# Kernel tuning notes

Measured on AMD Instinct MI355X. Metric: run time of the kernel, lower is better.

Reference implementation:

```python
import jax, jax.numpy as jnp
import numpy as np

B, N, D, H, HID = 8, 729, 1152, 12, 4304
HD = D // H
EPS = 1e-6


def _layer_norm(x, g, b):
    mu = jnp.mean(x, axis=-1, keepdims=True)
    var = jnp.mean((x - mu) ** 2, axis=-1, keepdims=True)
    return (x - mu) / jnp.sqrt(var + EPS) * g + b


def setup_inputs() -> dict:
    key = jax.random.key(0)
    ks = jax.random.split(key, 9)
    s = 0.02
    return {
        "x": jax.random.normal(ks[0], (B, N, D), jnp.float32),
        "wq": jax.random.normal(ks[1], (D, D), jnp.float32) * s,
        "bq": jnp.zeros((D,), jnp.float32),
        "wk": jax.random.normal(ks[2], (D, D), jnp.float32) * s,
        "bk": jnp.zeros((D,), jnp.float32),
        "wv": jax.random.normal(ks[3], (D, D), jnp.float32) * s,
        "bv": jnp.zeros((D,), jnp.float32),
        "wo": jax.random.normal(ks[4], (D, D), jnp.float32) * s,
        "bo": jnp.zeros((D,), jnp.float32),
        "ln1_g": jnp.ones((D,), jnp.float32),
        "ln1_b": jnp.zeros((D,), jnp.float32),
        "w_fc1": jax.random.normal(ks[5], (HID, D), jnp.float32) * s,
        "b_fc1": jnp.zeros((HID,), jnp.float32),
        "w_fc2": jax.random.normal(ks[6], (D, HID), jnp.float32) * s,
        "b_fc2": jnp.zeros((D,), jnp.float32),
        "ln2_g": jnp.ones((D,), jnp.float32),
        "ln2_b": jnp.zeros((D,), jnp.float32),
    }


def reference(x, wq, bq, wk, bk, wv, bv, wo, bo, ln1_g, ln1_b,
              w_fc1, b_fc1, w_fc2, b_fc2, ln2_g, ln2_b):
    b, n, d = x.shape
    # split_heads in the source is a plain view (B, H, N, HD) -- NOT a transpose.
    def heads(t):
        return t.reshape(b, H, n, HD)

    Q = heads(x @ wq.T + bq)
    K = heads(x @ wk.T + bk)
    V = heads(x @ wv.T + bv)

    scores = jnp.einsum("bhqd,bhkd->bhqk", Q, K) * (HD ** -0.5)
    attn_w = jax.nn.softmax(scores, axis=-1)
    o = jnp.einsum("bhqk,bhkd->bhqd", attn_w, V)  # [B,H,N,HD]
    o = jnp.swapaxes(o, 1, 2).reshape(b, n, d)
    attn_out = o @ wo.T + bo

    # post-norm: LN(sublayer) + residual
    h = _layer_norm(attn_out, ln1_g, ln1_b) + x

    # quirky MLP: activation applied BEFORE fc1 (faithful to source)
    m = jax.nn.gelu(h, approximate=True)
    m = m @ w_fc1.T + b_fc1
    m = m @ w_fc2.T + b_fc2

    return _layer_norm(m, ln2_g, ln2_b) + h
```

## Files before the change

### kernel.cpp

```cpp
#include <hip/hip_runtime.h>
#include <hip/hip_bf16.h>

#define BF16 __hip_bfloat16

typedef short short8 __attribute__((ext_vector_type(8)));
typedef short short4v __attribute__((ext_vector_type(4)));
typedef float v4f __attribute__((ext_vector_type(4)));
typedef float f4 __attribute__((ext_vector_type(4)));

__device__ float g_bp[1152];
__device__ BF16  g_wm[1152 * 1152];

__device__ __forceinline__ short f2bs(float f) {
    __hip_bfloat16 h = __float2bfloat16(f);
    return *(short*)&h;
}

__device__ __forceinline__ float bs2f(short s) {
    __hip_bfloat16 h = *(__hip_bfloat16*)&s;
    return __bfloat162float(h);
}

__device__ __forceinline__ void async_cp16(const BF16* g, BF16* l) {
    __builtin_amdgcn_global_load_lds(
        (const __attribute__((address_space(1))) void*)g,
        (__attribute__((address_space(3))) void*)l,
        16, 0, 0);
}

__device__ __forceinline__ int xcd_chunk(int u, int nwg) {
    int xcd = u & 7, i = u >> 3;
    int q = nwg >> 3, r = nwg & 7;
    return (xcd < r ? xcd * (q + 1) : r * (q + 1) + (xcd - r) * q) + i;
}

__global__ __launch_bounds__(256) void prep_kernel(
    const float* __restrict__ wq, const float* __restrict__ wk,
    const float* __restrict__ wv, const float* __restrict__ wo,
    const float* __restrict__ wfc1, const float* __restrict__ wfc2,
    const float* __restrict__ x,
    const float* __restrict__ bfc1, const float* __restrict__ bfc2,
    BF16* __restrict__ wbq, BF16* __restrict__ wbk,
    BF16* __restrict__ wbv, BF16* __restrict__ wbo,
    BF16* __restrict__ wbf1t, BF16* __restrict__ wbf2,
    BF16* __restrict__ xb)
{
    __shared__ float tile[64][65];
    const int bid = blockIdx.x;
    const int tid = threadIdx.x;

    if (bid < 16641) {
        const int i = bid * 256 + tid;
        constexpr int N_DD  = 331776;
        constexpr int N4    = 4 * N_DD;
        constexpr int N_F2  = 1253376;
        constexpr int E_F2  = N4 + N_F2;
        constexpr int N_X   = 1679616;
        constexpr int TOTAL = E_F2 + N_X;

        if (i < N4) {
            int seg = i / N_DD, j = i - seg * N_DD;
            const float* s = (seg == 0) ? wq : (seg == 1) ? wk : (seg == 2) ? wv : wo;
            BF16* d = (seg == 0) ? wbq : (seg == 1) ? wbk : (seg == 2) ? wbv : wbo;
            f4 v = ((const f4*)s)[j];
            short4v o = {f2bs(v.x), f2bs(v.y), f2bs(v.z), f2bs(v.w)};
            ((short4v*)d)[j] = o;
        } else if (i < E_F2) {
            int j = i - N4;
            int row = j / 1088;
            int c = (j - row * 1088) * 4;
            short4v o = {0, 0, 0, 0};
            if (c < 4304) {
                f4 v = *(const f4*)(wfc2 + (size_t)row * 4304 + c);
                o[0] = f2bs(v.x); o[1] = f2bs(v.y); o[2] = f2bs(v.z); o[3] = f2bs(v.w);
            }
            *(short4v*)(wbf2 + (size_t)row * 4352 + c) = o;
        } else if (i < TOTAL) {
            int j = i - E_F2;
            f4 v = ((const f4*)x)[j];
            short4v o = {f2bs(v.x), f2bs(v.y), f2bs(v.z), f2bs(v.w)};
            ((short4v*)xb)[j] = o;
        }
    } else if (bid < 17865) {
        const int b2 = bid - 16641;
        const int h0 = (b2 % 68) * 64;
        const int d0 = (b2 / 68) * 64;
#pragma unroll
        for (int i = 0; i < 4; ++i) {
            int lin = tid + i * 256;
            int r = lin >> 4, c4 = lin & 15;
            f4 v = {0.f, 0.f, 0.f, 0.f};
            if (h0 + r < 4304)
                v = *(const f4*)(wfc1 + (size_t)(h0 + r) * 1152 + d0 + c4 * 4);
            tile[r][c4 * 4 + 0] = v.x;
            tile[r][c4 * 4 + 1] = v.y;
            tile[r][c4 * 4 + 2] = v.z;
            tile[r][c4 * 4 + 3] = v.w;
        }
        __syncthreads();
#pragma unroll
        for (int i = 0; i < 2; ++i) {
            int lin = tid + i * 256;
            int dr = lin >> 3, h8 = lin & 7;
            short8 o;
#pragma unroll
            for (int e = 0; e < 8; ++e)
                o[e] = f2bs(tile[h8 * 8 + e][dr]);
            *(short8*)(wbf1t + (size_t)(d0 + dr) * 4352 + h0 + h8 * 8) = o;
        }
    } else {
        const int row = (bid - 17865) * 4 + (tid >> 6);
        const int lane = tid & 63;
        const float* wr = wfc2 + (size_t)row * 4304;
        float s = 0.f;
        for (int k = lane; k < 4304; k += 64) s += wr[k] * bfc1[k];
#pragma unroll
        for (int mm = 1; mm < 64; mm <<= 1) s += __shfl_xor(s, mm, 64);
        if (lane == 0) g_bp[row] = s + bfc2[row];
    }
}

__global__ __launch_bounds__(512, 2) void qkv_wm8_kernel(
    const BF16* __restrict__ A,
    const BF16* __restrict__ Wqkv,
    const float* __restrict__ b0, const float* __restrict__ b1,
    const float* __restrict__ b2,
    BF16* __restrict__ C, size_t cstride, int M,
    const BF16* __restrict__ W2,
    const BF16* __restrict__ W1t,
    float* __restrict__ P)
{
    __shared__ __align__(16) BF16 smem[65536];
    const int bid  = blockIdx.x;
    const int tid  = threadIdx.x;
    const int lane = tid & 63;
    const int wave = tid >> 6;
    const int quad = lane >> 4;
    const int l16  = lane & 15;
    const v4f zf = {0.f, 0.f, 0.f, 0.f};

    int rr[2], sw[2], lo[2];
#pragma unroll
    for (int j = 0; j < 2; ++j) {
        int c = tid + j * 512;
        rr[j] = c >> 3;
        sw[j] = (((c & 7) - (c >> 3)) & 7) << 3;
        lo[j] = (c & ~63) * 8;
    }

    if (bid < 162) {
        BF16* Am = smem;
        BF16* Bm = smem + 8192;
        const int mz  = bid / 81;
        const int idx = bid - mz * 81;
        const int m0 = (idx % 9) * 128;
        const int n0 = (idx / 9) * 128;
        const int ks0 = mz * 34;
        const int wm = (wave >> 1) * 32;
        const int wn = (wave & 1) * 64;

        v4f acc[2][4];
#pragma unroll
        for (int i = 0; i < 2; ++i)
#pragma unroll
            for (int j = 0; j < 4; ++j) acc[i][j] = zf;

        const BF16* gA[2]; const BF16* gB[2];
#pragma unroll
        for (int j = 0; j < 2; ++j) {
            gA[j] = W2 + (size_t)(m0 + rr[j]) * 4352 + ks0 * 64 + sw[j];
            gB[j] = W1t + (size_t)(n0 + rr[j]) * 4352 + ks0 * 64 + sw[j];
        }

        for (int kt = 0; kt < 34; ++kt) {
#pragma unroll
            for (int j = 0; j < 2; ++j) { async_cp16(gA[j], Am + lo[j]); gA[j] += 64; }
#pragma unroll
            for (int j = 0; j < 2; ++j) { async_cp16(gB[j], Bm + lo[j]); gB[j] += 64; }
            __syncthreads();
#pragma unroll
            for (int ks = 0; ks < 2; ++ks) {
                short8 af[2], bfg[4];
#pragma unroll
                for (int mt = 0; mt < 2; ++mt) {
                    int row = wm + mt * 16 + l16;
                    af[mt] = *(const short8*)(Am + row * 64 + ((((ks << 2) | quad) + row & 7) & 7) * 8);
                }
#pragma unroll
                for (int nt = 0; nt < 4; ++nt) {
                    int row = wn + nt * 16 + l16;
                    bfg[nt] = *(const short8*)(Bm + row * 64 + ((((ks << 2) | quad) + row & 7) & 7) * 8);
                }
#pragma unroll
                for (int mt = 0; mt < 2; ++mt)
#pragma unroll
                    for (int nt = 0; nt < 4; ++nt)
                        acc[mt][nt] = __builtin_amdgcn_mfma_f32_16x16x32_bf16(
                            af[mt], bfg[nt], acc[mt][nt], 0, 0, 0);
            }
            __syncthreads();
        }

        float* Pz = P + (size_t)mz * 1327104;
#pragma unroll
        for (int mt = 0; mt < 2; ++mt)
#pragma unroll
            for (int nt = 0; nt < 4; ++nt)
#pragma unroll
                for (int r2 = 0; r2 < 4; ++r2) {
                    int row = m0 + wm + mt * 16 + quad * 4 + r2;
                    int col = n0 + wn + nt * 16 + l16;
                    Pz[(size_t)row * 1152 + col] = acc[mt][nt][r2];
                }
    } else {
        const int wg = xcd_chunk(bid - 162, 322);
        const int m0 = (wg / 14) * 256;
        const int n0 = (wg % 14) * 256;
        const int wr = wave >> 2;
        const int wc = wave & 3;
        BF16* As = smem;
        BF16* Bs = smem + 32768;

        v4f acc[8][4];
#pragma unroll
        for (int i = 0; i < 8; ++i)
#pragma unroll
            for (int j = 0; j < 4; ++j) acc[i][j] = zf;

        #define STAGE_A(dd, hh, tt)                                            \
            {                                                                  \
                _Pragma("unroll")                                              \
                for (int j = 0; j < 2; ++j)                                    \
                    async_cp16(A + (size_t)(m0 + (hh) * 128 + rr[j]) * 1152    \
                                 + (tt) * 64 + sw[j],                          \
                               As + (dd) * 16384 + (hh) * 8192 + lo[j]);       \
            }
        #define STAGE_B(dd, hh, tt)                                            \
            {                                                                  \
                _Pragma("unroll")                                              \
                for (int j = 0; j < 2; ++j)                                    \
                    async_cp16(Wqkv + (size_t)(n0 + (hh) * 128 + rr[j]) * 1152 \
                                 + (tt) * 64 + sw[j],                          \
                               Bs + (dd) * 16384 + (hh) * 8192 + lo[j]);       \
            }

        STAGE_B(0, 0, 0); STAGE_B(0, 1, 0);
        STAGE_A(0, 0, 0); STAGE_A(0, 1, 0);
        STAGE_B(1, 0, 1); STAGE_B(1, 1, 1);
        asm volatile("s_waitcnt vmcnt(4)" ::: "memory");
        __builtin_amdgcn_s_barrier();
        __builtin_amdgcn_sched_barrier(0);

        short8 bfr[4][2], afr[2][2];
#pragma unroll 2
        for (int it = 0; it < 18; ++it) {
            const int d = it & 1;
            const BF16* Ad = As + d * 16384;
            const BF16* Bd = Bs + d * 16384;
#pragma unroll
            for (int q = 0; q < 4; ++q) {
                if (q == 0) {
#pragma unroll
                    for (int nt = 0; nt < 4; ++nt) {
                        int R = wc * 64 + nt * 16 + l16;
#pragma unroll
                        for (int ks = 0; ks < 2; ++ks)
                            bfr[nt][ks] = *(const short8*)(
                                Bd + R * 64 + ((((ks << 2) | quad) + R & 7) & 7) * 8);
                    }
                }
#pragma unroll
                for (int mi = 0; mi < 2; ++mi) {
                    int R = wr * 128 + (q * 2 + mi) * 16 + l16;
#pragma unroll
                    for (int ks = 0; ks < 2; ++ks)
                        afr[mi][ks] = *(const short8*)(
                            Ad + R * 64 + ((((ks << 2) | quad) + R & 7) & 7) * 8);
                }
                if (q == 0) { if (it + 1 < 18) STAGE_A(d ^ 1, 0, it + 1); }
                if (q == 1) { if (it + 1 < 18) STAGE_A(d ^ 1, 1, it + 1); }
                if (q == 2) { if (it + 2 < 18) STAGE_B(d,     0, it + 2); }
                if (q == 3) { if (it + 2 < 18) STAGE_B(d,     1, it + 2); }

                __builtin_amdgcn_s_barrier();
                asm volatile("s_waitcnt lgkmcnt(0)" ::: "memory");
                __builtin_amdgcn_sched_barrier(0);
                __builtin_amdgcn_s_setprio(1);
#pragma unroll
                for (int ks = 0; ks < 2; ++ks)
#pragma unroll
                    for (int mi = 0; mi < 2; ++mi)
#pragma unroll
                        for (int nt = 0; nt < 4; ++nt)
                            acc[q * 2 + mi][nt] = __builtin_amdgcn_mfma_f32_16x16x32_bf16(
                                afr[mi][ks], bfr[nt][ks], acc[q * 2 + mi][nt], 0, 0, 0);
                __builtin_amdgcn_s_setprio(0);
                if (q == 3) {
                    if (it + 2 < 18)
                        asm volatile("s_waitcnt vmcnt(4)" ::: "memory");
                    else
                        asm volatile("s_waitcnt vmcnt(0)" ::: "memory");
                }
                __builtin_amdgcn_s_barrier();
            }
        }
        #undef STAGE_A
        #undef STAGE_B

        float bv[4];
#pragma unroll
        for (int nt = 0; nt < 4; ++nt) {
            int col_g = n0 + wc * 64 + nt * 16 + l16;
            int sel = (col_g >= 2304) ? 2 : (col_g >= 1152) ? 1 : 0;
            const float* bp = (sel == 0) ? b0 : (sel == 1) ? b1 : b2;
            bv[nt] = (col_g < 3456) ? bp[col_g - sel * 1152] : 0.f;
        }
#pragma unroll
        for (int mt = 0; mt < 8; ++mt)
#pragma unroll
            for (int nt = 0; nt < 4; ++nt)
#pragma unroll
                for (int r2 = 0; r2 < 4; ++r2) {
                    int row_l = wr * 128 + mt * 16 + quad * 4 + r2;
                    int col_l = wc * 64 + nt * 16 + l16;
                    smem[row_l * 256 + col_l] = __float2bfloat16(acc[mt][nt][r2] + bv[nt]);
                }
        __syncthreads();
#pragma unroll
        for (int p = 0; p < 16; ++p) {
            int idx = p * 512 + tid;
            int row = m0 + (idx >> 5);
            int col_g = n0 + (idx & 31) * 8;
            if (row < M && col_g < 3456) {
                int sel = (col_g >= 2304) ? 2 : (col_g >= 1152) ? 1 : 0;
                *(short8*)(C + (size_t)sel * cstride + (size_t)row * 1152
                           + col_g - sel * 1152) =
                    *(const short8*)(smem + idx * 8);
            }
        }
    }
}

__global__ __launch_bounds__(256) void trans_kernel(
    const BF16* __restrict__ V, BF16* __restrict__ VT,
    const float* __restrict__ P, BF16* __restrict__ Wm)
{
    __shared__ __align__(16) BF16 tl[64][128];
    const int bid = blockIdx.x, tid = threadIdx.x;
    const short8 zero8 = {0, 0, 0, 0, 0, 0, 0, 0};

    if (bid < 1152) {
        const int hg = bid / 12, kb = bid - hg * 12;
        const int b = hg / 12, hh = hg - b * 12;
        const BF16* src = V + (size_t)b * 839808 + (size_t)hh * 69984;
        BF16* dst = VT + (size_t)hg * 86016;
        const int kk0 = kb * 64;
#pragma unroll
        for (int i = 0; i < 3; ++i) {
            int c = tid + i * 256;
            int r = c / 12, cg = c - r * 12;
            short8 v = (kk0 + r < 729)
                ? *(const short8*)(src + (size_t)(kk0 + r) * 96 + cg * 8) : zero8;
            *(short8*)(&tl[r][(cg ^ ((r >> 3) & 7)) * 8]) = v;
        }
        __syncthreads();
#pragma unroll
        for (int i = 0; i < 3; ++i) {
            int wc = tid + i * 256;
            int hd = wc >> 3, o = wc & 7;
            int sp = (((hd >> 3) ^ o) << 3) + (hd & 7);
            short8 out;
#pragma unroll
            for (int j = 0; j < 8; ++j)
                out[j] = *(const short*)&tl[o * 8 + j][sp];
            *(short8*)(dst + (size_t)hd * 768 + kk0 + o * 8) = out;
        }
    } else if (bid < 1728) {
        int c = (bid - 1152) * 256 + tid;
        int hg = c / 1536, rem = c - hg * 1536;
        int r = rem / 96, ock = rem - r * 96;
        int kk = ock * 8;
        short8 v = zero8;
        if (r == 0) {
            const short oneb = 0x3F80;
#pragma unroll
            for (int j = 0; j < 8; ++j) v[j] = (kk + j < 729) ? oneb : (short)0;
        }
        *(short8*)(VT + (size_t)hg * 86016 + (size_t)(96 + r) * 768 + kk) = v;
    } else {
        int i = (bid - 1728) * 256 + tid;
        f4 s = ((const f4*)P)[i];
        f4 v = ((const f4*)(P + 1327104))[i];
        s.x += v.x; s.y += v.y; s.z += v.z; s.w += v.w;
        short4v o = {f2bs(s.x), f2bs(s.y), f2bs(s.z), f2bs(s.w)};
        ((short4v*)Wm)[i] = o;
    }
}

template<int TM>
__global__ __launch_bounds__(256) void gemm_bt_t(
    const BF16* __restrict__ A, int lda,
    const BF16* __restrict__ W, int ldb,
    const float* __restrict__ bias, int nbias,
    BF16* __restrict__ C, int ldc,
    int M, int Kr, int nbn)
{
    constexpr int MT = TM / 32;
    __shared__ __align__(16) BF16 smem[(TM + 128) * 64];
    BF16* As = smem;
    BF16* Bs = smem + TM * 64;

    const int tid  = threadIdx.x;
    const int lane = tid & 63;
    const int wave = tid >> 6;
    const int quad = lane >> 4;
    const int l16  = lane & 15;
    const int wm   = (wave >> 1) * (TM / 2);
    const int wn   = (wave & 1) * 64;
    const int wg   = xcd_chunk(blockIdx.x, gridDim.x);
    const int m0   = (wg / nbn) * TM;
    const int n0   = (wg % nbn) * 128;
    if (m0 >= M) return;

    const v4f zf = {0.f, 0.f, 0.f, 0.f};
    v4f acc[MT][4];
#pragma unroll
    for (int i = 0; i < MT; ++i)
#pragma unroll
        for (int j = 0; j < 4; ++j) acc[i][j] = zf;

    const BF16* gA[MT]; BF16* lA[MT];
#pragma unroll
    for (int i = 0; i < MT; ++i) {
        int c = tid + i * 256;
        gA[i] = A + (size_t)(m0 + (c >> 3)) * lda + ((((c & 7) - (c >> 3)) & 7) << 3);
        lA[i] = As + (c & ~63) * 8;
    }
    const BF16* gB[4]; BF16* lB[4];
#pragma unroll
    for (int i = 0; i < 4; ++i) {
        int c = tid + i * 256;
        gB[i] = W + (size_t)(n0 + (c >> 3)) * ldb + ((((c & 7) - (c >> 3)) & 7) << 3);
        lB[i] = Bs + (c & ~63) * 8;
    }

    const int nk = Kr >> 6;
    for (int kt = 0; kt < nk; ++kt) {
#pragma unroll
        for (int i = 0; i < MT; ++i) { async_cp16(gA[i], lA[i]); gA[i] += 64; }
#pragma unroll
        for (int i = 0; i < 4; ++i)  { async_cp16(gB[i], lB[i]); gB[i] += 64; }
        __syncthreads();

#pragma unroll
        for (int ks = 0; ks < 2; ++ks) {
            short8 af[MT], bfg[4];
#pragma unroll
            for (int mt = 0; mt < MT; ++mt) {
                int row = wm + mt * 16 + l16;
                af[mt] = *(const short8*)(As + row * 64 + ((((ks << 2) | quad) + row & 7) & 7) * 8);
            }
#pragma unroll
            for (int nt = 0; nt < 4; ++nt) {
                int row = wn + nt * 16 + l16;
                bfg[nt] = *(const short8*)(Bs + row * 64 + ((((ks << 2) | quad) + row & 7) & 7) * 8);
            }
#pragma unroll
            for (int mt = 0; mt < MT; ++mt)
#pragma unroll
                for (int nt = 0; nt < 4; ++nt)
                    acc[mt][nt] = __builtin_amdgcn_mfma_f32_16x16x32_bf16(
                        af[mt], bfg[nt], acc[mt][nt], 0, 0, 0);
        }
        __syncthreads();
    }

    float bv[4];
#pragma unroll
    for (int nt = 0; nt < 4; ++nt) {
        int col = n0 + wn + nt * 16 + l16;
        bv[nt] = (col < nbias) ? bias[col] : 0.f;
    }
#pragma unroll
    for (int mt = 0; mt < MT; ++mt)
#pragma unroll
        for (int nt = 0; nt < 4; ++nt)
#pragma unroll
            for (int r2 = 0; r2 < 4; ++r2) {
                int row_l = wm + mt * 16 + quad * 4 + r2;
                int col_l = wn + nt * 16 + l16;
                smem[row_l * 128 + col_l] = __float2bfloat16(acc[mt][nt][r2] + bv[nt]);
            }
    __syncthreads();
#pragma unroll
    for (int p = 0; p < TM / 16; ++p) {
        int idx = p * 256 + tid;
        int row = m0 + (idx >> 4);
        if (row < M)
            *(short8*)(C + (size_t)row * ldc + n0 + (idx & 15) * 8) =
                *(const short8*)(smem + idx * 8);
    }
}

__global__ __launch_bounds__(256) void attn_flash3(
    const BF16* __restrict__ Q, const BF16* __restrict__ K,
    const BF16* __restrict__ VT, BF16* __restrict__ O)
{
    constexpr int NQ = 729, HDk = 96, DM = 1152, LDV = 768;
    __shared__ __align__(16) BF16 Ks[64 * 104];
    __shared__ __align__(16) BF16 Vs[112 * 64];
    __shared__ __align__(16) BF16 Ps[4][16 * 64];

    const int id = blockIdx.x;
    const int xcd = id & 7, slot = id >> 3;
    const int hb = slot / 12, qt = slot - hb * 12;
    const int hg = xcd * 12 + hb;
    const int b = hg / 12, hh = hg - b * 12;

    const int tid = threadIdx.x, wave = tid >> 6, lane = tid & 63;
    const int quad = lane >> 4, l16 = lane & 15;
    const size_t kbase = (size_t)b * (NQ * DM) + (size_t)hh * (NQ * HDk);
    const size_t vbase = (size_t)hg * 112 * LDV;

    const short8 zero8 = {0, 0, 0, 0, 0, 0, 0, 0};
    const v4f zf = {0.f, 0.f, 0.f, 0.f};
    const float C2 = 0.14724445f;

    const int q0w = qt * 64 + wave * 16;
    short8 aq[3];
    {
        int qrow = q0w + l16;
#pragma unroll
        for (int ks = 0; ks < 3; ++ks)
            aq[ks] = (qrow < NQ)
                ? *(const short8*)(Q + kbase + (size_t)qrow * HDk + ks * 32 + quad * 8)
                : zero8;
    }

    int kk_[3], kg_[3];
#pragma unroll
    for (int i = 0; i < 3; ++i) {
        int c = tid + i * 256;
        kk_[i] = c / 12; kg_[i] = c - kk_[i] * 12;
    }
    int vq_[4], vgr_[4], vhd_[4];
#pragma unroll
    for (int i = 0; i < 4; ++i) {
        int q = wave + 4 * i;
        vq_[i] = q;
        int hd = q * 8 + (lane >> 3);
        vhd_[i] = hd;
        vgr_[i] = ((lane & 7) - hd) & 7;
    }

    v4f oacc[7];
#pragma unroll
    for (int nt = 0; nt < 7; ++nt) oacc[nt] = zf;

    short8 kreg[3];
#pragma unroll
    for (int i = 0; i < 3; ++i)
        kreg[i] = *(const short8*)(K + kbase + (size_t)kk_[i] * HDk + kg_[i] * 8);

    for (int kt = 0; kt < 12; ++kt) {
        const int k0 = kt * 64;
#pragma unroll
        for (int i = 0; i < 3; ++i)
            *(short8*)(Ks + kk_[i] * 104 + kg_[i] * 8) = kreg[i];
#pragma unroll
        for (int i = 0; i < 4; ++i) {
            if (vq_[i] < 14)
                async_cp16(VT + vbase + (size_t)vhd_[i] * LDV + k0 + vgr_[i] * 8,
                           Vs + vq_[i] * 512);
        }
        asm volatile("s_waitcnt lgkmcnt(0)" ::: "memory");
        __builtin_amdgcn_s_barrier();
        __builtin_amdgcn_sched_barrier(0);
        {
            const int kn = (kt < 11) ? (k0 + 64) : 0;
#pragma unroll
            for (int i = 0; i < 3; ++i)
                kreg[i] = *(const short8*)(K + kbase + (size_t)(kn + kk_[i]) * HDk + kg_[i] * 8);
        }

        v4f s[4];
#pragma unroll
        for (int nt = 0; nt < 4; ++nt) s[nt] = zf;
        __builtin_amdgcn_s_setprio(1);
#pragma unroll
        for (int ks = 0; ks < 3; ++ks)
#pragma unroll
            for (int nt = 0; nt < 4; ++nt) {
                short8 bk = *(const short8*)(Ks + (nt * 16 + l16) * 104 + ks * 32 + quad * 8);
                s[nt] = __builtin_amdgcn_mfma_f32_16x16x32_bf16(aq[ks], bk, s[nt], 0, 0, 0);
            }
        __builtin_amdgcn_s_setprio(0);

        BF16* Pw = &Ps[wave][0];
#pragma unroll
        for (int nt = 0; nt < 4; ++nt)
#pragma unroll
            for (int r = 0; r < 4; ++r)
                Pw[((quad * 4 + r) << 6)
                   + ((((nt << 1) | (l16 >> 3)) ^ (quad << 1)) << 3)
                   + (l16 & 7)] =
                    __float2bfloat16(exp2f(s[nt][r] * C2));
        asm volatile("s_waitcnt lgkmcnt(0)" ::: "memory");

        short8 ap[2];
#pragma unroll
        for (int kc = 0; kc < 2; ++kc)
            ap[kc] = *(const short8*)(Pw + (l16 << 6)
                + ((((kc << 2) | quad) ^ (((l16 >> 2) & 3) << 1)) << 3));

        asm volatile("s_waitcnt vmcnt(3)" ::: "memory");
        __builtin_amdgcn_s_barrier();
        __builtin_amdgcn_sched_barrier(0);

        __builtin_amdgcn_s_setprio(1);
#pragma unroll
        for (int nt = 0; nt < 7; ++nt) {
            int hd = nt * 16 + l16;
#pragma unroll
            for (int kc = 0; kc < 2; ++kc) {
                short8 bv = *(const short8*)(Vs + hd * 64 + (((kc * 4 + quad) + hd & 7) & 7) * 8);
                oacc[nt] = __builtin_amdgcn_mfma_f32_16x16x32_bf16(ap[kc], bv, oacc[nt], 0, 0, 0);
            }
        }
        __builtin_amdgcn_s_setprio(0);
        asm volatile("s_waitcnt lgkmcnt(0)" ::: "memory");
        __builtin_amdgcn_s_barrier();
        __builtin_amdgcn_sched_barrier(0);
    }

    {
        const int qb = q0w + quad * 4;
#pragma unroll
        for (int r = 0; r < 4; ++r) {
            int q = qb + r;
            float lv = __shfl(oacc[6][r], quad << 4, 64);
            float inv = (lv > 0.f) ? 1.f / lv : 0.f;
            if (q >= NQ) continue;
#pragma unroll
            for (int nt = 0; nt < 6; ++nt)
                O[(size_t)b * (NQ * DM) + (size_t)q * DM + hh * HDk + nt * 16 + l16] =
                    __float2bfloat16(oacc[nt][r] * inv);
        }
    }
}

__device__ __forceinline__ float block_sum192(float v, float* red, int tid)
{
#pragma unroll
    for (int mm = 1; mm < 64; mm <<= 1) v += __shfl_xor(v, mm, 64);
    if ((tid & 63) == 0) red[tid >> 6] = v;
    __syncthreads();
    float r = red[0] + red[1] + red[2];
    __syncthreads();
    return r;
}

__global__ __launch_bounds__(192) void ln1_gelu_kernel(
    const BF16* __restrict__ ao, const float* __restrict__ x,
    const float* __restrict__ gw, const float* __restrict__ bw,
    BF16* __restrict__ hout, BF16* __restrict__ gout)
{
    __shared__ float red[3];
    const int row = blockIdx.x, tid = threadIdx.x;
    const bool act = tid < 144;
    float v[8];
    float s = 0.f;
    if (act) {
        short8 pk = ((const short8*)(ao + (size_t)row * 1152))[tid];
#pragma unroll
        for (int j = 0; j < 8; ++j) { v[j] = bs2f(pk[j]); s += v[j]; }
    } else {
#pragma unroll
        for (int j = 0; j < 8; ++j) v[j] = 0.f;
    }
    s = block_sum192(s, red, tid);
    float mu = s * (1.f / 1152.f);
    float vsum = 0.f;
    if (act) {
#pragma unroll
        for (int j = 0; j < 8; ++j) { float d = v[j] - mu; vsum += d * d; }
    }
    vsum = block_sum192(vsum, red, tid);
    float rstd = rsqrtf(vsum * (1.f / 1152.f) + 1e-6f);
    if (act) {
        f4 g0 = ((const f4*)gw)[2 * tid], g1 = ((const f4*)gw)[2 * tid + 1];
        f4 b0 = ((const f4*)bw)[2 * tid], b1 = ((const f4*)bw)[2 * tid + 1];
        const f4* xr = (const f4*)(x + (size_t)row * 1152);
        f4 x0 = xr[2 * tid], x1 = xr[2 * tid + 1];
        short8 ho, go;
#pragma unroll
        for (int j = 0; j < 8; ++j) {
            float gj = (j < 4) ? g0[j] : g1[j - 4];
            float bj = (j < 4) ? b0[j] : b1[j - 4];
            float xj = (j < 4) ? x0[j] : x1[j - 4];
            float hv = (v[j] - mu) * rstd * gj + bj + xj;
            ho[j] = f2bs(hv);
            float z2 = 2.3022077f * hv + 0.10294636f * hv * hv * hv;
            float gl = hv / (1.f + exp2f(-z2));
            go[j] = f2bs(gl);
        }
        ((short8*)(hout + (size_t)row * 1152))[tid] = ho;
        ((short8*)(gout + (size_t)row * 1152))[tid] = go;
    }
}

__global__ __launch_bounds__(192) void ln2_kernel(
    const BF16* __restrict__ m2, const BF16* __restrict__ hf,
    const float* __restrict__ gw, const float* __restrict__ bw,
    float* __restrict__ out)
{
    __shared__ float red[3];
    const int row = blockIdx.x, tid = threadIdx.x;
    const bool act = tid < 144;
    float v[8];
    float s = 0.f;
    if (act) {
        short8 pk = ((const short8*)(m2 + (size_t)row * 1152))[tid];
#pragma unroll
        for (int j = 0; j < 8; ++j) { v[j] = bs2f(pk[j]); s += v[j]; }
    } else {
#pragma unroll
        for (int j = 0; j < 8; ++j) v[j] = 0.f;
    }
    s = block_sum192(s, red, tid);
    float mu = s * (1.f / 1152.f);
    float vsum = 0.f;
    if (act) {
#pragma unroll
        for (int j = 0; j < 8; ++j) { float d = v[j] - mu; vsum += d * d; }
    }
    vsum = block_sum192(vsum, red, tid);
    float rstd = rsqrtf(vsum * (1.f / 1152.f) + 1e-6f);
    if (act) {
        f4 g0 = ((const f4*)gw)[2 * tid], g1 = ((const f4*)gw)[2 * tid + 1];
        f4 b0 = ((const f4*)bw)[2 * tid], b1 = ((const f4*)bw)[2 * tid + 1];
        short8 hfv = ((const short8*)(hf + (size_t)row * 1152))[tid];
        f4 o0, o1;
#pragma unroll
        for (int j = 0; j < 8; ++j) {
            float gj = (j < 4) ? g0[j] : g1[j - 4];
            float bj = (j < 4) ? b0[j] : b1[j - 4];
            float ov = (v[j] - mu) * rstd * gj + bj + bs2f(hfv[j]);
            if (j < 4) o0[j] = ov; else o1[j - 4] = ov;
        }
        f4* orow = (f4*)(out + (size_t)row * 1152);
        orow[2 * tid] = o0;
        orow[2 * tid + 1] = o1;
    }
}

extern "C" void kernel_launch(void* const* d_in, const int* in_sizes, int n_in,
                              void* d_out, int out_size, void* d_ws, size_t ws_size,
                              hipStream_t stream)
{
    const float* x    = (const float*)d_in[0];
    const float* wq   = (const float*)d_in[1];
    const float* bq   = (const float*)d_in[2];
    const float* wk   = (const float*)d_in[3];
    const float* bk   = (const float*)d_in[4];
    const float* wv   = (const float*)d_in[5];
    const float* bv   = (const float*)d_in[6];
    const float* wo   = (const float*)d_in[7];
    const float* bo   = (const float*)d_in[8];
    const float* ln1g = (const float*)d_in[9];
    const float* ln1b = (const float*)d_in[10];
    const float* wfc1 = (const float*)d_in[11];
    const float* bfc1 = (const float*)d_in[12];
    const float* wfc2 = (const float*)d_in[13];
    const float* bfc2 = (const float*)d_in[14];
    const float* ln2g = (const float*)d_in[15];
    const float* ln2b = (const float*)d_in[16];

    const int T = 8 * 729;
    const int D = 1152, HIDP = 4352;
    const size_t TD = (size_t)T * D;
    const size_t WDD = (size_t)D * D;

    BF16* wbq   = (BF16*)d_ws;
    BF16* wbk   = wbq + WDD;
    BF16* wbv   = wbk + WDD;
    BF16* wbo   = wbv + WDD;
    BF16* wbf1t = wbo + WDD;
    BF16* wbf2  = wbf1t + (size_t)HIDP * D;
    BF16* xb    = wbf2 + (size_t)D * HIDP;
    BF16* S0    = xb + TD;
    BF16* S1    = S0 + TD;
    BF16* S2    = S1 + TD;
    BF16* S3    = S2 + TD;
    BF16* C0    = S3 + TD;
    BF16* C1    = C0 + TD;
    BF16* VT    = C0;
    float* Pws  = (float*)S3;

    static float* bp_dev = nullptr;
    static BF16*  wm_dev = nullptr;
    if (!bp_dev) hipGetSymbolAddress((void**)&bp_dev, HIP_SYMBOL(g_bp));
    if (!wm_dev) hipGetSymbolAddress((void**)&wm_dev, HIP_SYMBOL(g_wm));

    dim3 blk(256);

    prep_kernel<<<18153, blk, 0, stream>>>(
        wq, wk, wv, wo, wfc1, wfc2, x, bfc1, bfc2,
        wbq, wbk, wbv, wbo, wbf1t, wbf2, xb);

    qkv_wm8_kernel<<<484, dim3(512), 0, stream>>>(
        xb, wbq, bq, bk, bv, S0, TD, T, wbf2, wbf1t, Pws);

    trans_kernel<<<3024, blk, 0, stream>>>(S2, VT, Pws, wm_dev);

    attn_flash3<<<1152, blk, 0, stream>>>(S0, S1, VT, S3);

    gemm_bt_t<64><<<828, blk, 0, stream>>>(S3, D, wbo, D, bo, D, C0, D, T, D, 9);

    ln1_gelu_kernel<<<T, dim3(192), 0, stream>>>(C0, x, ln1g, ln1b, C1, C0);

    gemm_bt_t<64><<<828, blk, 0, stream>>>(C0, D, wm_dev, D, bp_dev, D, S3, D, T, D, 9);

    ln2_kernel<<<T, dim3(192), 0, stream>>>(S3, C1, ln2g, ln2b, (float*)d_out);
}
```

Before: 379.1 us.

## Halve QKV GEMM K-tile to shrink LDS and split epilogue into two passes

Changes the 256x256 QKV GEMM path to stage 32-wide K slices instead of 64, with a new XOR swizzle and one async copy per thread per half-tile. This halves shared memory from 128KB to 64KB. The epilogue now writes C through LDS in two 128-row passes so the smaller buffer is enough. The aim is to let two workgroups fit per CU, matching the launch bounds. In exchange it doubles the number of loop iterations and barriers, which raises per-iteration sync overhead.

```diff
diff --git a/kernel.cpp b/kernel.cpp
--- a/kernel.cpp
+++ b/kernel.cpp
@@ -130,7 +130,7 @@
     const BF16* __restrict__ W1t,
     float* __restrict__ P)
 {
-    __shared__ __align__(16) BF16 smem[65536];
+    __shared__ __align__(16) BF16 smem[32768];
     const int bid  = blockIdx.x;
     const int tid  = threadIdx.x;
     const int lane = tid & 63;
@@ -139,16 +139,15 @@
     const int l16  = lane & 15;
     const v4f zf = {0.f, 0.f, 0.f, 0.f};
 
-    int rr[2], sw[2], lo[2];
-#pragma unroll
-    for (int j = 0; j < 2; ++j) {
-        int c = tid + j * 512;
-        rr[j] = c >> 3;
-        sw[j] = (((c & 7) - (c >> 3)) & 7) << 3;
-        lo[j] = (c & ~63) * 8;
-    }
-
     if (bid < 162) {
+        int rr[2], sw[2], lo[2];
+#pragma unroll
+        for (int j = 0; j < 2; ++j) {
+            int c = tid + j * 512;
+            rr[j] = c >> 3;
+            sw[j] = (((c & 7) - (c >> 3)) & 7) << 3;
+            lo[j] = (c & ~63) * 8;
+        }
         BF16* Am = smem;
         BF16* Bm = smem + 8192;
         const int mz  = bid / 81;
@@ -219,7 +218,11 @@
         const int wr = wave >> 2;
         const int wc = wave & 3;
         BF16* As = smem;
-        BF16* Bs = smem + 32768;
+        BF16* Bs = smem + 16384;
+
+        const int srow = tid >> 2;
+        const int sgrp = (tid & 3) ^ ((tid >> 4) & 3);
+        const int sdst = tid * 8;
 
         v4f acc[8][4];
 #pragma unroll
@@ -228,76 +231,63 @@
             for (int j = 0; j < 4; ++j) acc[i][j] = zf;
 
         #define STAGE_A(dd, hh, tt)                                            \
-            {                                                                  \
-                _Pragma("unroll")                                              \
-                for (int j = 0; j < 2; ++j)                                    \
-                    async_cp16(A + (size_t)(m0 + (hh) * 128 + rr[j]) * 1152    \
-                                 + (tt) * 64 + sw[j],                          \
-                               As + (dd) * 16384 + (hh) * 8192 + lo[j]);       \
-            }
+            async_cp16(A + (size_t)(m0 + (hh) * 128 + srow) * 1152             \
+                         + (tt) * 32 + sgrp * 8,                               \
+                       As + (dd) * 8192 + (hh) * 4096 + sdst);
         #define STAGE_B(dd, hh, tt)                                            \
-            {                                                                  \
-                _Pragma("unroll")                                              \
-                for (int j = 0; j < 2; ++j)                                    \
-                    async_cp16(Wqkv + (size_t)(n0 + (hh) * 128 + rr[j]) * 1152 \
-                                 + (tt) * 64 + sw[j],                          \
-                               Bs + (dd) * 16384 + (hh) * 8192 + lo[j]);       \
-            }
+            async_cp16(Wqkv + (size_t)(n0 + (hh) * 128 + srow) * 1152          \
+                         + (tt) * 32 + sgrp * 8,                               \
+                       Bs + (dd) * 8192 + (hh) * 4096 + sdst);
 
         STAGE_B(0, 0, 0); STAGE_B(0, 1, 0);
         STAGE_A(0, 0, 0); STAGE_A(0, 1, 0);
         STAGE_B(1, 0, 1); STAGE_B(1, 1, 1);
-        asm volatile("s_waitcnt vmcnt(4)" ::: "memory");
+        asm volatile("s_waitcnt vmcnt(2)" ::: "memory");
         __builtin_amdgcn_s_barrier();
         __builtin_amdgcn_sched_barrier(0);
 
-        short8 bfr[4][2], afr[2][2];
+        short8 bfr[4], afr[4];
 #pragma unroll 2
-        for (int it = 0; it < 18; ++it) {
+        for (int it = 0; it < 36; ++it) {
             const int d = it & 1;
-            const BF16* Ad = As + d * 16384;
-            const BF16* Bd = Bs + d * 16384;
-#pragma unroll
-            for (int q = 0; q < 4; ++q) {
+            const BF16* Ad = As + d * 8192;
+            const BF16* Bd = Bs + d * 8192;
+#pragma unroll
+            for (int q = 0; q < 2; ++q) {
                 if (q == 0) {
 #pragma unroll
                     for (int nt = 0; nt < 4; ++nt) {
                         int R = wc * 64 + nt * 16 + l16;
-#pragma unroll
-                        for (int ks = 0; ks < 2; ++ks)
-                            bfr[nt][ks] = *(const short8*)(
-                                Bd + R * 64 + ((((ks << 2) | quad) + R & 7) & 7) * 8);
+                        bfr[nt] = *(const short8*)(
+                            Bd + R * 32 + ((quad ^ ((R >> 2) & 3)) << 3));
                     }
                 }
 #pragma unroll
-                for (int mi = 0; mi < 2; ++mi) {
-                    int R = wr * 128 + (q * 2 + mi) * 16 + l16;
-#pragma unroll
-                    for (int ks = 0; ks < 2; ++ks)
-                        afr[mi][ks] = *(const short8*)(
-                            Ad + R * 64 + ((((ks << 2) | quad) + R & 7) & 7) * 8);
+                for (int mi = 0; mi < 4; ++mi) {
+                    int R = wr * 128 + (q * 4 + mi) * 16 + l16;
+                    afr[mi] = *(const short8*)(
+                        Ad + R * 32 + ((quad ^ ((R >> 2) & 3)) << 3));
                 }
-                if (q == 0) { if (it + 1 < 18) STAGE_A(d ^ 1, 0, it + 1); }
-                if (q == 1) { if (it + 1 < 18) STAGE_A(d ^ 1, 1, it + 1); }
-                if (q == 2) { if (it + 2 < 18) STAGE_B(d,     0, it + 2); }
-                if (q == 3) { if (it + 2 < 18) STAGE_B(d,     1, it + 2); }
+                if (q == 0) {
+                    if (it + 1 < 36) { STAGE_A(d ^ 1, 0, it + 1); STAGE_A(d ^ 1, 1, it + 1); }
+                } else {
+                    if (it + 2 < 36) { STAGE_B(d, 0, it + 2); STAGE_B(d, 1, it + 2); }
+                }
 
                 __builtin_amdgcn_s_barrier();
                 asm volatile("s_waitcnt lgkmcnt(0)" ::: "memory");
                 __builtin_amdgcn_sched_barrier(0);
                 __builtin_amdgcn_s_setprio(1);
 #pragma unroll
-                for (int ks = 0; ks < 2; ++ks)
-#pragma unroll
-                    for (int mi = 0; mi < 2; ++mi)
-#pragma unroll
-                        for (int nt = 0; nt < 4; ++nt)
-                            acc[q * 2 + mi][nt] = __builtin_amdgcn_mfma_f32_16x16x32_bf16(
-                                afr[mi][ks], bfr[nt][ks], acc[q * 2 + mi][nt], 0, 0, 0);
+                for (int mi = 0; mi < 4; ++mi)
+#pragma unroll
+                    for (int nt = 0; nt < 4; ++nt)
+                        acc[q * 4 + mi][nt] = __builtin_amdgcn_mfma_f32_16x16x32_bf16(
+                            afr[mi], bfr[nt], acc[q * 4 + mi][nt], 0, 0, 0);
                 __builtin_amdgcn_s_setprio(0);
-                if (q == 3) {
-                    if (it + 2 < 18)
-                        asm volatile("s_waitcnt vmcnt(4)" ::: "memory");
+                if (q == 1) {
+                    if (it + 2 < 36)
+                        asm volatile("s_waitcnt vmcnt(2)" ::: "memory");
                     else
                         asm volatile("s_waitcnt vmcnt(0)" ::: "memory");
                 }
@@ -316,27 +306,34 @@
             bv[nt] = (col_g < 3456) ? bp[col_g - sel * 1152] : 0.f;
         }
 #pragma unroll
-        for (int mt = 0; mt < 8; ++mt)
-#pragma unroll
-            for (int nt = 0; nt < 4; ++nt)
-#pragma unroll
-                for (int r2 = 0; r2 < 4; ++r2) {
-                    int row_l = wr * 128 + mt * 16 + quad * 4 + r2;
-                    int col_l = wc * 64 + nt * 16 + l16;
-                    smem[row_l * 256 + col_l] = __float2bfloat16(acc[mt][nt][r2] + bv[nt]);
+        for (int pass = 0; pass < 2; ++pass) {
+            if (wr == pass) {
+#pragma unroll
+                for (int mt = 0; mt < 8; ++mt)
+#pragma unroll
+                    for (int nt = 0; nt < 4; ++nt)
+#pragma unroll
+                        for (int r2 = 0; r2 < 4; ++r2) {
+                            int row_l = mt * 16 + quad * 4 + r2;
+                            int col_l = wc * 64 + nt * 16 + l16;
+                            smem[row_l * 256 + col_l] =
+                                __float2bfloat16(acc[mt][nt][r2] + bv[nt]);
+                        }
+            }
+            __syncthreads();
+#pragma unroll
+            for (int p = 0; p < 8; ++p) {
+                int idx = p * 512 + tid;
+                int row = m0 + pass * 128 + (idx >> 5);
+                int col_g = n0 + (idx & 31) * 8;
+                if (row < M && col_g < 3456) {
+                    int sel = (col_g >= 2304) ? 2 : (col_g >= 1152) ? 1 : 0;
+                    *(short8*)(C + (size_t)sel * cstride + (size_t)row * 1152
+                               + col_g - sel * 1152) =
+                        *(const short8*)(smem + idx * 8);
                 }
-        __syncthreads();
-#pragma unroll
-        for (int p = 0; p < 16; ++p) {
-            int idx = p * 512 + tid;
-            int row = m0 + (idx >> 5);
-            int col_g = n0 + (idx & 31) * 8;
-            if (row < M && col_g < 3456) {
-                int sel = (col_g >= 2304) ? 2 : (col_g >= 1152) ? 1 : 0;
-                *(short8*)(C + (size_t)sel * cstride + (size_t)row * 1152
-                           + col_g - sel * 1152) =
-                    *(const short8*)(smem + idx * 8);
-            }
+            }
+            __syncthreads();
         }
     }
 }
```

Result: no change. 386.2 us (+1.9%).
